# Performance work log

Measured on AMD Instinct MI355X. Metric: run time of the kernel, lower is better.

## Reference

```python
import jax, jax.numpy as jnp
import numpy as np
from jax import lax

START_TAG_IDX = 1
NUM_TAGS = 64
END_TAG_IDX = NUM_TAGS - 1
NEG_INF = -10000.0


def _forward_alg(feats, mask, transitions):
    # feats: (B, S, N), mask: (B, S) float, transitions: (N, N)
    B, S, N = feats.shape
    init = jnp.full((B, N), NEG_INF, dtype=feats.dtype).at[:, START_TAG_IDX].set(0.0)

    def step(fv, xs):
        emit, m = xs  # (B, N), (B,)
        # logsumexp over previous tag: fv[b, prev] + T[prev, next]
        nv = jax.nn.logsumexp(fv[:, :, None] + transitions[None, :, :], axis=1) + emit
        m = m[:, None]
        fv = m * nv + (1.0 - m) * fv
        return fv, None

    fv, _ = lax.scan(step, init, (jnp.swapaxes(feats, 0, 1), mask.T))
    terminal = fv + transitions[:, END_TAG_IDX][None, :]
    return jax.nn.logsumexp(terminal, axis=1)  # (B,)


def _score_sentence(feats, mask, tags, transitions):
    B, S, N = feats.shape
    start = jnp.full((B, 1), START_TAG_IDX, dtype=tags.dtype)
    tags_ext = jnp.concatenate([start, tags], axis=1)  # (B, S+1)
    # emission score at gold tags, masked
    emit = jnp.take_along_axis(feats, tags[:, :, None], axis=2)[:, :, 0]  # (B, S)
    # transition score tags[i] -> tags[i+1], masked
    trans = transitions[tags_ext[:, :-1], tags_ext[:, 1:]]  # (B, S)
    score = jnp.sum((emit + trans) * mask, axis=1)
    # transition from last real tag to END
    seq_ends = mask.sum(axis=1).astype(jnp.int32) - 1  # (B,)
    last_tags = tags_ext[jnp.arange(B), seq_ends + 1]
    return score + transitions[last_tags, END_TAG_IDX]


def reference(feats, mask, tags, transitions):
    forward_score = _forward_alg(feats, mask, transitions)
    gold_score = _score_sentence(feats, mask, tags, transitions)
    return jnp.mean(forward_score - gold_score)  # average_batch=True


def setup_inputs() -> dict:
    key = jax.random.key(0)
    k1, k2, k3 = jax.random.split(key, 3)
    B, S, N = 512, 512, NUM_TAGS
    feats = jax.random.normal(k1, (B, S, N), dtype=jnp.float32)
    mask = jnp.ones((B, S), dtype=jnp.float32)
    tags = jax.random.randint(k2, (B, S), 0, N).astype(jnp.int64)
    transitions = jax.random.uniform(k3, (N, N), dtype=jnp.float32, minval=-0.1, maxval=0.1)
    return {"feats": feats, "mask": mask, "tags": tags, "transitions": transitions}
```

## Files before the change

kernel.cpp:

```cpp
#include <hip/hip_runtime.h>
#include <hip/hip_bf16.h>

#define NTAGS 64
#define START_TAG 1
#define END_TAG 63
#define LN2F 0.69314718055994530942f
#define NSEG 32

typedef float v4f __attribute__((ext_vector_type(4)));
typedef short s16x8 __attribute__((ext_vector_type(8)));

static __device__ __forceinline__ unsigned short f2bfu(float x) {
    union { __hip_bfloat16 h; unsigned short s; } u;
    u.h = __float2bfloat16(x);
    return u.s;
}
static __device__ __forceinline__ unsigned int packbf(float lo, float hi) {
    return (unsigned int)f2bfu(lo) | ((unsigned int)f2bfu(hi) << 16);
}
static __device__ __forceinline__ float xor16_get(float send) {
    auto rr = __builtin_amdgcn_permlane16_swap(__float_as_uint(send), __float_as_uint(send),
                                               false, false);
    return (__uint_as_float((unsigned)rr[0]) + __uint_as_float((unsigned)rr[1])) - send;
}
static __device__ __forceinline__ float xor32_get(float send) {
    auto rr = __builtin_amdgcn_permlane32_swap(__float_as_uint(send), __float_as_uint(send),
                                               false, false);
    return (__uint_as_float((unsigned)rr[0]) + __uint_as_float((unsigned)rr[1])) - send;
}
static __device__ __forceinline__ v4f max4(v4f a, v4f b) {
    return __builtin_elementwise_max(a, b);
}

template <bool FWD>
static __device__ __forceinline__ void run_seg_mfma(
    const float* __restrict__ feats, const float* __restrict__ mask,
    const float* __restrict__ trans, float* __restrict__ outv,
    int* __restrict__ oute, int S, int t_begin, int L, int b0, int init_mode) {
    const int lane = threadIdx.x & 63;
    const int c = lane & 15, g = lane >> 4;

    s16x8 Af[4][2];
#pragma unroll
    for (int m = 0; m < 4; ++m)
#pragma unroll
        for (int kk = 0; kk < 2; ++kk)
#pragma unroll
            for (int e = 0; e < 8; ++e) {
                float tv = FWD ? trans[(32 * kk + 8 * g + e) * NTAGS + 16 * m + c]
                               : trans[(16 * m + c) * NTAGS + 32 * kk + 8 * g + e];
                Af[m][kk][e] = (short)f2bfu(__expf(tv));
            }

    v4f D[4];
    if (init_mode == 0) {
#pragma unroll
        for (int m = 0; m < 4; ++m) D[m] = (v4f){0.f, 0.f, 0.f, 0.f};
        if (g == 0) D[0].y = 1.0f;
    } else if (init_mode == 1) {
#pragma unroll
        for (int m = 0; m < 4; ++m) D[m] = (v4f){1.f, 1.f, 1.f, 1.f};
    } else {
#pragma unroll
        for (int m = 0; m < 4; ++m) {
            D[m].x = __expf(trans[(16 * m + 4 * g + 0) * NTAGS + END_TAG]);
            D[m].y = __expf(trans[(16 * m + 4 * g + 1) * NTAGS + END_TAG]);
            D[m].z = __expf(trans[(16 * m + 4 * g + 2) * NTAGS + END_TAG]);
            D[m].w = __expf(trans[(16 * m + 4 * g + 3) * NTAGS + END_TAG]);
        }
    }

    const float* fb = feats + (size_t)(b0 + c) * S * NTAGS;
    const float* mb = mask + (size_t)(b0 + c) * S;
    int esum = 0;

#define TT(sv) (FWD ? (t_begin + (sv)) : (t_begin + L - 1 - (sv)))
#define ELOAD(Ereg, Mreg, sv)                                                     \
    do {                                                                          \
        _Pragma("unroll") for (int n = 0; n < 4; ++n)                             \
            Ereg[n] = *(const v4f*)(fb + (size_t)TT(sv) * NTAGS + 16 * n + 4 * g);\
        Mreg = mb[TT(sv)];                                                        \
    } while (0)

#define STEPX(Ereg, Mv)                                                           \
    do {                                                                          \
        v4f Ex[4];                                                               \
        _Pragma("unroll") for (int n = 0; n < 4; ++n) {                           \
            Ex[n].x = __expf(Ereg[n].x); Ex[n].y = __expf(Ereg[n].y);             \
            Ex[n].z = __expf(Ereg[n].z); Ex[n].w = __expf(Ereg[n].w);             \
        }                                                                         \
        unsigned int up[4][2];                                                    \
        _Pragma("unroll") for (int n = 0; n < 4; ++n) {                           \
            v4f sv = FWD ? D[n] : D[n] * Ex[n];                                   \
            up[n][0] = packbf(sv.x, sv.y);                                        \
            up[n][1] = packbf(sv.z, sv.w);                                        \
        }                                                                         \
        union { unsigned int d[4]; s16x8 v; } bf0, bf1;                           \
        {                                                                         \
            auto rA = __builtin_amdgcn_permlane32_swap(up[0][0], up[1][0], false, false); \
            auto rB = __builtin_amdgcn_permlane32_swap(up[0][1], up[1][1], false, false); \
            auto rC = __builtin_amdgcn_permlane32_swap(up[2][0], up[3][0], false, false); \
            auto rD = __builtin_amdgcn_permlane32_swap(up[2][1], up[3][1], false, false); \
            auto sA = __builtin_amdgcn_permlane16_swap((unsigned)rA[0], (unsigned)rA[1], false, false); \
            auto sB = __builtin_amdgcn_permlane16_swap((unsigned)rB[0], (unsigned)rB[1], false, false); \
            auto sC = __builtin_amdgcn_permlane16_swap((unsigned)rC[0], (unsigned)rC[1], false, false); \
            auto sD = __builtin_amdgcn_permlane16_swap((unsigned)rD[0], (unsigned)rD[1], false, false); \
            bf0.d[0] = sA[0]; bf0.d[1] = sB[0]; bf0.d[2] = sA[1]; bf0.d[3] = sB[1]; \
            bf1.d[0] = sC[0]; bf1.d[1] = sD[0]; bf1.d[2] = sC[1]; bf1.d[3] = sD[1]; \
        }                                                                         \
        v4f Dm[4];                                                                \
        _Pragma("unroll") for (int m = 0; m < 4; ++m) {                           \
            v4f z = (v4f){0.f, 0.f, 0.f, 0.f};                                    \
            Dm[m] = __builtin_amdgcn_mfma_f32_16x16x32_bf16(Af[m][0], bf0.v, z, 0, 0, 0); \
            Dm[m] = __builtin_amdgcn_mfma_f32_16x16x32_bf16(Af[m][1], bf1.v, Dm[m], 0, 0, 0); \
        }                                                                         \
        if (FWD) {                                                                \
            _Pragma("unroll") for (int m = 0; m < 4; ++m) Dm[m] = Dm[m] * Ex[m];  \
        }                                                                         \
        bool act = (Mv != 0.0f);                                                  \
        _Pragma("unroll") for (int m = 0; m < 4; ++m) D[m] = act ? Dm[m] : D[m];  \
    } while (0)

    v4f EA[4], EB[4], EC[4], ED[4];
    float MA, MB, MC, MD;
    ELOAD(EA, MA, 0);
    ELOAD(EB, MB, 1);

    for (int s = 0; s < L; s += 4) {
        ELOAD(EC, MC, s + 2);
        ELOAD(ED, MD, s + 3);
        STEPX(EA, MA);
        STEPX(EB, MB);
        if (s + 4 < L) {
            ELOAD(EA, MA, s + 4);
            ELOAD(EB, MB, s + 5);
        }
        STEPX(EC, MC);
        STEPX(ED, MD);
        if (((s + 4) & 7) == 0) {
            v4f mm = max4(max4(D[0], D[1]), max4(D[2], D[3]));
            float mx = fmaxf(fmaxf(mm.x, mm.y), fmaxf(mm.z, mm.w));
            mx = fmaxf(mx, xor16_get(mx));
            mx = fmaxf(mx, xor32_get(mx));
            int ex;
            (void)frexpf(mx, &ex);
#pragma unroll
            for (int m = 0; m < 4; ++m) {
                D[m].x = ldexpf(D[m].x, -ex);
                D[m].y = ldexpf(D[m].y, -ex);
                D[m].z = ldexpf(D[m].z, -ex);
                D[m].w = ldexpf(D[m].w, -ex);
            }
            esum += ex;
        }
    }
#undef STEPX
#undef ELOAD
#undef TT

    float* oc = outv + (size_t)(b0 + c) * NTAGS;
#pragma unroll
    for (int m = 0; m < 4; ++m) *(v4f*)(oc + 16 * m + 4 * g) = D[m];
    if (g == 0) oute[b0 + c] = esum;
}

__global__ __launch_bounds__(64) void crf_chains(const float* __restrict__ feats,
                                                 const float* __restrict__ mask,
                                                 const int* __restrict__ tags,
                                                 const float* __restrict__ trans,
                                                 float* __restrict__ seg,
                                                 int* __restrict__ es,
                                                 float* __restrict__ gs,
                                                 int S, int L, int B, int nchain) {
    const int bid = (int)blockIdx.x;
    const int lane = threadIdx.x;

    if (bid >= nchain) {
        const int b = bid - nchain;
        const float* fb = feats + (size_t)b * S * NTAGS;
        const float* mb = mask + (size_t)b * S;
        const int* tb = tags + (size_t)b * S;
        float acc = 0.f, msum = 0.f;
        for (int t = lane; t < S; t += 64) {
            int cur = tb[t];
            int prev = (t == 0) ? START_TAG : tb[t - 1];
            float m = mb[t];
            acc += (fb[t * NTAGS + cur] + trans[prev * NTAGS + cur]) * m;
            msum += m;
        }
#pragma unroll
        for (int sh = 32; sh >= 1; sh >>= 1) {
            acc += __shfl_xor(acc, sh);
            msum += __shfl_xor(msum, sh);
        }
        if (lane == 0) {
            int seq_end = (int)(msum + 0.5f) - 1;
            int last = (seq_end >= 0) ? tb[seq_end] : START_TAG;
            gs[b] = acc + trans[last * NTAGS + END_TAG];
        }
        return;
    }

    const int ngrp = B / 16;
    const int type = bid / ngrp;
    const int grp = bid - type * ngrp;
    const int b0 = grp * 16;

    float* outv = seg + (size_t)type * B * NTAGS;
    int* oute = es + type * B;

    if (type < 31) {
        run_seg_mfma<true>(feats, mask, trans, outv, oute, S, type * L, L, b0,
                           (type == 0) ? 0 : 1);
    } else {
        const int sg = type - 30;
        run_seg_mfma<false>(feats, mask, trans, outv, oute, S, sg * L, L, b0,
                            (sg == 31) ? 2 : 1);
    }
}

__global__ __launch_bounds__(512) void crf_finish(const float* __restrict__ seg,
                                                  const int* __restrict__ es,
                                                  const float* __restrict__ gs,
                                                  float* __restrict__ scores, int B) {
    const int tid = threadIdx.x;
    const int wave = tid >> 6, lane = tid & 63;
    const int b = blockIdx.x * 8 + wave;
    if (b >= B) return;

    float contrib = 0.f;
    if (lane < 31) {
        const int g = lane + 1;
        const float* rv = seg + ((size_t)(g - 1) * B + b) * NTAGS;
        const float* lv = seg + ((size_t)(30 + g) * B + b) * NTAGS;
        v4f dacc = (v4f){0.f, 0.f, 0.f, 0.f};
        v4f sacc = dacc;
#pragma unroll
        for (int i = 0; i < 16; ++i) {
            v4f rr = *(const v4f*)(rv + 4 * i);
            v4f ll = *(const v4f*)(lv + 4 * i);
            dacc = __builtin_elementwise_fma(ll, rr, dacc);
            sacc = sacc + ll;
        }
        float dot = (dacc.x + dacc.y) + (dacc.z + dacc.w);
        float sl = (sacc.x + sacc.y) + (sacc.z + sacc.w);
        contrib = __logf(dot) + (float)es[(size_t)(g - 1) * B + b] * LN2F;
        if (g <= 30) contrib -= __logf(sl);
    } else if (lane == 31) {
        contrib = (float)es[(size_t)61 * B + b] * LN2F;
    }
#pragma unroll
    for (int sh = 32; sh >= 1; sh >>= 1) contrib += __shfl_xor(contrib, sh);
    if (lane == 0) scores[b] = contrib - gs[b];
}

__global__ __launch_bounds__(1024) void crf_mean(const float* __restrict__ scores,
                                                 float* __restrict__ out, int B) {
    const int tid = threadIdx.x;
    float a = 0.f;
    for (int i = tid; i < B; i += 1024) a += scores[i];
#pragma unroll
    for (int sh = 32; sh >= 1; sh >>= 1) a += __shfl_xor(a, sh);
    __shared__ float buf[16];
    if ((tid & 63) == 0) buf[tid >> 6] = a;
    __syncthreads();
    if (tid == 0) {
        float s = 0.f;
#pragma unroll
        for (int i = 0; i < 16; ++i) s += buf[i];
        out[0] = s / (float)B;
    }
}

extern "C" void kernel_launch(void* const* d_in, const int* in_sizes, int n_in,
                              void* d_out, int out_size, void* d_ws, size_t ws_size,
                              hipStream_t stream) {
    const float* feats = (const float*)d_in[0];
    const float* mask  = (const float*)d_in[1];
    const int*   tags  = (const int*)d_in[2];
    const float* trans = (const float*)d_in[3];
    float* out = (float*)d_out;

    const int S = 512;
    const int B = in_sizes[1] / S;
    const int L = S / NSEG;
    const int nchain = 62 * (B / 16);

    float* seg = (float*)d_ws;
    int* es = (int*)(seg + (size_t)62 * B * NTAGS);
    float* gs = (float*)(es + 62 * B);
    float* scores = gs + B;

    crf_chains<<<nchain + B, 64, 0, stream>>>(feats, mask, tags, trans,
                                              seg, es, gs, S, L, B, nchain);
    crf_finish<<<(B + 7) / 8, 512, 0, stream>>>(seg, es, gs, scores, B);
    crf_mean<<<1, 1024, 0, stream>>>(scores, out, B);
}
```

Before: 42.63 us.

## Split chains into 64 segments, precompute exp(transitions) once, rescale only at end

```diff
diff --git a/kernel.cpp b/kernel.cpp
--- a/kernel.cpp
+++ b/kernel.cpp
@@ -5,7 +5,7 @@
 #define START_TAG 1
 #define END_TAG 63
 #define LN2F 0.69314718055994530942f
-#define NSEG 32
+#define NSEG 64
 
 typedef float v4f __attribute__((ext_vector_type(4)));
 typedef short s16x8 __attribute__((ext_vector_type(8)));
@@ -32,25 +32,45 @@
     return __builtin_elementwise_max(a, b);
 }
 
+__global__ __launch_bounds__(64) void crf_setup(const float* __restrict__ trans,
+                                                s16x8* __restrict__ afws,
+                                                float* __restrict__ uws) {
+    const int lane = threadIdx.x;
+    const int c = lane & 15, g = lane >> 4;
+#pragma unroll
+    for (int m = 0; m < 4; ++m)
+#pragma unroll
+        for (int kk = 0; kk < 2; ++kk) {
+            s16x8 vf, vb;
+#pragma unroll
+            for (int e = 0; e < 8; ++e) {
+                vf[e] = (short)f2bfu(__expf(trans[(32 * kk + 8 * g + e) * NTAGS + 16 * m + c]));
+                vb[e] = (short)f2bfu(__expf(trans[(16 * m + c) * NTAGS + 32 * kk + 8 * g + e]));
+            }
+            afws[(0 * 8 + 2 * m + kk) * 64 + lane] = vf;
+            afws[(1 * 8 + 2 * m + kk) * 64 + lane] = vb;
+        }
+    uws[lane] = __expf(trans[lane * NTAGS + END_TAG]);
+}
+
 template <bool FWD>
 static __device__ __forceinline__ void run_seg_mfma(
     const float* __restrict__ feats, const float* __restrict__ mask,
-    const float* __restrict__ trans, float* __restrict__ outv,
-    int* __restrict__ oute, int S, int t_begin, int L, int b0, int init_mode) {
+    const s16x8* __restrict__ afws, const float* __restrict__ uws,
+    float* __restrict__ outv, int* __restrict__ oute,
+    int S, int t_begin, int L, int b0, int init_mode) {
     const int lane = threadIdx.x & 63;
     const int c = lane & 15, g = lane >> 4;
 
     s16x8 Af[4][2];
-#pragma unroll
-    for (int m = 0; m < 4; ++m)
-#pragma unroll
-        for (int kk = 0; kk < 2; ++kk)
-#pragma unroll
-            for (int e = 0; e < 8; ++e) {
-                float tv = FWD ? trans[(32 * kk + 8 * g + e) * NTAGS + 16 * m + c]
-                               : trans[(16 * m + c) * NTAGS + 32 * kk + 8 * g + e];
-                Af[m][kk][e] = (short)f2bfu(__expf(tv));
-            }
+    {
+        const s16x8* base = afws + (FWD ? 0 : 8) * 64;
+#pragma unroll
+        for (int m = 0; m < 4; ++m)
+#pragma unroll
+            for (int kk = 0; kk < 2; ++kk)
+                Af[m][kk] = base[(2 * m + kk) * 64 + lane];
+    }
 
     v4f D[4];
     if (init_mode == 0) {
@@ -62,12 +82,7 @@
         for (int m = 0; m < 4; ++m) D[m] = (v4f){1.f, 1.f, 1.f, 1.f};
     } else {
 #pragma unroll
-        for (int m = 0; m < 4; ++m) {
-            D[m].x = __expf(trans[(16 * m + 4 * g + 0) * NTAGS + END_TAG]);
-            D[m].y = __expf(trans[(16 * m + 4 * g + 1) * NTAGS + END_TAG]);
-            D[m].z = __expf(trans[(16 * m + 4 * g + 2) * NTAGS + END_TAG]);
-            D[m].w = __expf(trans[(16 * m + 4 * g + 3) * NTAGS + END_TAG]);
-        }
+        for (int m = 0; m < 4; ++m) D[m] = *(const v4f*)(uws + 16 * m + 4 * g);
     }
 
     const float* fb = feats + (size_t)(b0 + c) * S * NTAGS;
@@ -84,7 +99,7 @@
 
 #define STEPX(Ereg, Mv)                                                           \
     do {                                                                          \
-        v4f Ex[4];                                                               \
+        v4f Ex[4];                                                                \
         _Pragma("unroll") for (int n = 0; n < 4; ++n) {                           \
             Ex[n].x = __expf(Ereg[n].x); Ex[n].y = __expf(Ereg[n].y);             \
             Ex[n].z = __expf(Ereg[n].z); Ex[n].w = __expf(Ereg[n].w);             \
@@ -137,13 +152,19 @@
         }
         STEPX(EC, MC);
         STEPX(ED, MD);
-        if (((s + 4) & 7) == 0) {
-            v4f mm = max4(max4(D[0], D[1]), max4(D[2], D[3]));
-            float mx = fmaxf(fmaxf(mm.x, mm.y), fmaxf(mm.z, mm.w));
-            mx = fmaxf(mx, xor16_get(mx));
-            mx = fmaxf(mx, xor32_get(mx));
-            int ex;
-            (void)frexpf(mx, &ex);
+    }
+#undef STEPX
+#undef ELOAD
+#undef TT
+
+    {
+        v4f mm = max4(max4(D[0], D[1]), max4(D[2], D[3]));
+        float mx = fmaxf(fmaxf(mm.x, mm.y), fmaxf(mm.z, mm.w));
+        mx = fmaxf(mx, xor16_get(mx));
+        mx = fmaxf(mx, xor32_get(mx));
+        int ef = (__float_as_int(mx) >> 23) & 0xFF;
+        if (ef != 0) {
+            int ex = ef - 127;
 #pragma unroll
             for (int m = 0; m < 4; ++m) {
                 D[m].x = ldexpf(D[m].x, -ex);
@@ -151,12 +172,9 @@
                 D[m].z = ldexpf(D[m].z, -ex);
                 D[m].w = ldexpf(D[m].w, -ex);
             }
-            esum += ex;
-        }
-    }
-#undef STEPX
-#undef ELOAD
-#undef TT
+            esum = ex;
+        }
+    }
 
     float* oc = outv + (size_t)(b0 + c) * NTAGS;
 #pragma unroll
@@ -168,6 +186,8 @@
                                                  const float* __restrict__ mask,
                                                  const int* __restrict__ tags,
                                                  const float* __restrict__ trans,
+                                                 const s16x8* __restrict__ afws,
+                                                 const float* __restrict__ uws,
                                                  float* __restrict__ seg,
                                                  int* __restrict__ es,
                                                  float* __restrict__ gs,
@@ -209,13 +229,13 @@
     float* outv = seg + (size_t)type * B * NTAGS;
     int* oute = es + type * B;
 
-    if (type < 31) {
-        run_seg_mfma<true>(feats, mask, trans, outv, oute, S, type * L, L, b0,
+    if (type < 63) {
+        run_seg_mfma<true>(feats, mask, afws, uws, outv, oute, S, type * L, L, b0,
                            (type == 0) ? 0 : 1);
     } else {
-        const int sg = type - 30;
-        run_seg_mfma<false>(feats, mask, trans, outv, oute, S, sg * L, L, b0,
-                            (sg == 31) ? 2 : 1);
+        const int sg = type - 62;
+        run_seg_mfma<false>(feats, mask, afws, uws, outv, oute, S, sg * L, L, b0,
+                            (sg == 63) ? 2 : 1);
     }
 }
 
@@ -229,10 +249,10 @@
     if (b >= B) return;
 
     float contrib = 0.f;
-    if (lane < 31) {
+    if (lane < 63) {
         const int g = lane + 1;
         const float* rv = seg + ((size_t)(g - 1) * B + b) * NTAGS;
-        const float* lv = seg + ((size_t)(30 + g) * B + b) * NTAGS;
+        const float* lv = seg + ((size_t)(62 + g) * B + b) * NTAGS;
         v4f dacc = (v4f){0.f, 0.f, 0.f, 0.f};
         v4f sacc = dacc;
 #pragma unroll
@@ -245,9 +265,9 @@
         float dot = (dacc.x + dacc.y) + (dacc.z + dacc.w);
         float sl = (sacc.x + sacc.y) + (sacc.z + sacc.w);
         contrib = __logf(dot) + (float)es[(size_t)(g - 1) * B + b] * LN2F;
-        if (g <= 30) contrib -= __logf(sl);
-    } else if (lane == 31) {
-        contrib = (float)es[(size_t)61 * B + b] * LN2F;
+        if (g <= 62) contrib -= __logf(sl);
+    } else {
+        contrib = (float)es[(size_t)125 * B + b] * LN2F;
     }
 #pragma unroll
     for (int sh = 32; sh >= 1; sh >>= 1) contrib += __shfl_xor(contrib, sh);
@@ -284,14 +304,18 @@
     const int S = 512;
     const int B = in_sizes[1] / S;
     const int L = S / NSEG;
-    const int nchain = 62 * (B / 16);
-
-    float* seg = (float*)d_ws;
-    int* es = (int*)(seg + (size_t)62 * B * NTAGS);
-    float* gs = (float*)(es + 62 * B);
+    const int nchain = 126 * (B / 16);
+
+    float* afws = (float*)d_ws;
+    float* uws = afws + 4096;
+    float* seg = uws + 64;
+    int* es = (int*)(seg + (size_t)126 * B * NTAGS);
+    float* gs = (float*)(es + 126 * B);
     float* scores = gs + B;
 
+    crf_setup<<<1, 64, 0, stream>>>(trans, (s16x8*)afws, uws);
     crf_chains<<<nchain + B, 64, 0, stream>>>(feats, mask, tags, trans,
+                                              (const s16x8*)afws, uws,
                                               seg, es, gs, S, L, B, nchain);
     crf_finish<<<(B + 7) / 8, 512, 0, stream>>>(seg, es, gs, scores, B);
     crf_mean<<<1, 1024, 0, stream>>>(scores, out, B);
```

New measurement: 51.16 us. 1.2x slower.
